# Kernel optimization log

Hardware: AMD Instinct MI355X
Metric: run time of the kernel (lower is better)

## Reference

```python
import jax, jax.numpy as jnp
import numpy as np

B, D, C, F = 1024, 8192, 345, 512
PROTO_W = 0.99  # args.proto_m


def setup_inputs() -> dict:
    key = jax.random.key(0)
    k = jax.random.split(key, 6)
    img_q = jax.random.normal(k[0], (B, D), jnp.float32)
    img_q1 = jax.random.normal(k[1], (B, D), jnp.float32)
    # partial label mask: random candidate set, guarantee >=1 candidate per row
    partial_Y = (jax.random.uniform(k[2], (B, C)) < 0.3).astype(jnp.float32)
    partial_Y = partial_Y.at[jnp.arange(B), jnp.arange(B) % C].set(1.0)
    W_enc = jax.random.normal(k[3], (D, F), jnp.float32) / np.sqrt(D).astype(np.float32)
    W_fc = jax.random.normal(k[4], (F, C), jnp.float32) / np.sqrt(F).astype(np.float32)
    b_fc = jnp.zeros((C,), jnp.float32)
    proto = jax.random.normal(k[5], (C, F), jnp.float32)
    proto = proto / jnp.linalg.norm(proto, axis=1, keepdims=True)
    return {"img_q": img_q, "img_q1": img_q1, "partial_Y": partial_Y,
            "W_enc": W_enc, "W_fc": W_fc, "b_fc": b_fc, "proto": proto}


def reference(img_q, img_q1, partial_Y, W_enc, W_fc, b_fc, proto):
    # encoder: feats [B,F], logits [B,C] (abstracted backbone + shared fc)
    feats_q = img_q @ W_enc
    logits_q = feats_q @ W_fc + b_fc
    feats_q1 = img_q1 @ W_enc
    logits_q1 = feats_q1 @ W_fc + b_fc

    # partial-label restricted pseudo labels
    scores = jax.nn.softmax(logits_q, axis=1) * partial_Y
    scores = scores / scores.sum(axis=1, keepdims=True)
    labels = jnp.argmax(scores, axis=1)  # [B] int

    # Sequential per-sample EMA p[l] = w*p[l] + (1-w)*f, vectorized in closed form.
    # For a sample with c_after same-label samples occurring later, its final
    # contribution is (1-w)*w^c_after * f; the old prototype is scaled by w^count.
    onehot = jax.nn.one_hot(labels, C, dtype=feats_q.dtype)   # [B,C]
    cum = jnp.cumsum(onehot, axis=0)                          # inclusive counts
    occ = cum[jnp.arange(B), labels] - 1.0                    # occurrences before i
    total = cum[-1]                                           # [C] per-class counts
    c_after = total[labels] - occ - 1.0                       # [B]
    coef = (1.0 - PROTO_W) * PROTO_W ** c_after               # [B]
    contrib = jax.ops.segment_sum(coef[:, None] * feats_q, labels, num_segments=C)
    new_proto = (PROTO_W ** total)[:, None] * proto + contrib
    new_proto = new_proto / jnp.linalg.norm(new_proto, axis=1, keepdims=True)

    prot_scores = new_proto @ W_fc + b_fc
    return logits_q, logits_q1, new_proto, prot_scores, labels, feats_q, feats_q1
```

## Files before the change

### kernel.cpp

```cpp
#include <hip/hip_runtime.h>
#include <float.h>
#include <math.h>

#define B_SZ 1024
#define D_SZ 8192
#define C_SZ 345
#define F_SZ 512
#define PROTO_W 0.99f


#define WS_XH 0
#define WS_XL 33554432u
#define WS_WH 67108864u
#define WS_WL 75497472u
#define WS_P  83886080u
#define WS2_WFH 100663296u
#define WS2_WFL 101056512u
#define WS2_LAB 101449728u
#define WS2_NEED 101457920u
#define WS2_FH 0u
#define WS2_FL 2097152u

#define WS_NEED 92274688u
#define WS_FH  0u
#define WS_FL  2097152u
#define WS_WFH 4194304u
#define WS_WFL 4587520u
#define WS_NPH 4980736u
#define WS_NPL 5373952u

typedef short bf16x8 __attribute__((ext_vector_type(8)));
typedef short short4v __attribute__((ext_vector_type(4)));
typedef short short8v __attribute__((ext_vector_type(8)));
typedef float f32x4  __attribute__((ext_vector_type(4)));

__device__ __forceinline__ void split_bf16(float x, short& hi, short& lo) {
    unsigned u = __float_as_uint(x);
    unsigned r = (u + 0x7FFFu + ((u >> 16) & 1u)) >> 16;
    hi = (short)r;
    float hf = __uint_as_float(r << 16);
    lo = (short)(__float_as_uint(x - hf) >> 16);
}
__device__ __forceinline__ float bf16_f32(short h) {
    return __uint_as_float(((unsigned)(unsigned short)h) << 16);
}

__device__ __forceinline__ void gl_lds16(const short* g, short* l) {
    __builtin_amdgcn_global_load_lds(
        (const __attribute__((address_space(1))) void*)g,
        (__attribute__((address_space(3))) void*)l, 16, 0, 0);
}

__device__ __forceinline__ unsigned f2key(float v) {
    unsigned u = __float_as_uint(v);
    return (u & 0x80000000u) ? ~u : (u | 0x80000000u);
}

__device__ __forceinline__ void fence_barrier() {
    asm volatile("" ::: "memory");
    __builtin_amdgcn_s_barrier();
    asm volatile("" ::: "memory");
}

#define MFMA_BF16 __builtin_amdgcn_mfma_f32_16x16x32_bf16

#define MFMA_BLOCK(IA0, IA1, IB0, IB1)                                   \
    do {                                                                 \
        bf16x8 a0h = *(const bf16x8*)&sAh[IA0];                          \
        bf16x8 a1h = *(const bf16x8*)&sAh[IA1];                          \
        bf16x8 b0h = *(const bf16x8*)&sBh[IB0];                          \
        bf16x8 b1h = *(const bf16x8*)&sBh[IB1];                          \
        bf16x8 a0l = *(const bf16x8*)&sAl[IA0];                          \
        bf16x8 a1l = *(const bf16x8*)&sAl[IA1];                          \
        bf16x8 b0l = *(const bf16x8*)&sBl[IB0];                          \
        bf16x8 b1l = *(const bf16x8*)&sBl[IB1];                          \
        acc[0][0] = MFMA_BF16(a0h, b0h, acc[0][0], 0, 0, 0);             \
        acc[0][1] = MFMA_BF16(a0h, b1h, acc[0][1], 0, 0, 0);             \
        acc[1][0] = MFMA_BF16(a1h, b0h, acc[1][0], 0, 0, 0);             \
        acc[1][1] = MFMA_BF16(a1h, b1h, acc[1][1], 0, 0, 0);             \
        acc[0][0] = MFMA_BF16(a0h, b0l, acc[0][0], 0, 0, 0);             \
        acc[0][1] = MFMA_BF16(a0h, b1l, acc[0][1], 0, 0, 0);             \
        acc[1][0] = MFMA_BF16(a1h, b0l, acc[1][0], 0, 0, 0);             \
        acc[1][1] = MFMA_BF16(a1h, b1l, acc[1][1], 0, 0, 0);             \
        acc[0][0] = MFMA_BF16(a0l, b0h, acc[0][0], 0, 0, 0);             \
        acc[0][1] = MFMA_BF16(a0l, b1h, acc[0][1], 0, 0, 0);             \
        acc[1][0] = MFMA_BF16(a1l, b0h, acc[1][0], 0, 0, 0);             \
        acc[1][1] = MFMA_BF16(a1l, b1h, acc[1][1], 0, 0, 0);             \
    } while (0)

__global__ __launch_bounds__(256) void convert_all(
    const float* __restrict__ img_q, const float* __restrict__ img_q1,
    const float* __restrict__ W_enc, const float* __restrict__ W_fc,
    short* __restrict__ Xh, short* __restrict__ Xl,
    short* __restrict__ Wh, short* __restrict__ Wl,
    short* __restrict__ Wth, short* __restrict__ Wtl)
{
    __shared__ float tile[64][65];
    const int bid = blockIdx.x;
    const int t = threadIdx.x;

    if (bid < 1024) {
        const int HALF = (B_SZ * D_SZ) / 4;
        const int total = 2 * HALF;
        for (int i4 = bid * 256 + t; i4 < total; i4 += 1024 * 256) {
            float4 v = (i4 < HALF) ? ((const float4*)img_q)[i4]
                                   : ((const float4*)img_q1)[i4 - HALF];
            short4v h, l;
            short hh, ll;
            split_bf16(v.x, hh, ll); h.x = hh; l.x = ll;
            split_bf16(v.y, hh, ll); h.y = hh; l.y = ll;
            split_bf16(v.z, hh, ll); h.z = hh; l.z = ll;
            split_bf16(v.w, hh, ll); h.w = hh; l.w = ll;
            ((short4v*)Xh)[i4] = h;
            ((short4v*)Xl)[i4] = l;
        }
    } else if (bid < 2048) {
        const int id = bid - 1024;
        const int k0 = (id >> 3) * 64;
        const int n0 = (id & 7) * 64;
        {
            const int kr = t >> 2;
            const int cb = (t & 3) * 16;
#pragma unroll
            for (int j = 0; j < 4; ++j) {
                float4 v = *(const float4*)&W_enc[(size_t)(k0 + kr) * F_SZ + n0 + cb + j * 4];
                tile[kr][cb + j * 4 + 0] = v.x;
                tile[kr][cb + j * 4 + 1] = v.y;
                tile[kr][cb + j * 4 + 2] = v.z;
                tile[kr][cb + j * 4 + 3] = v.w;
            }
        }
        __syncthreads();
        const int n = t >> 2;
#pragma unroll
        for (int cc = 0; cc < 2; ++cc) {
            const int ch = (t & 3) * 2 + cc;
            short8v h, l;
#pragma unroll
            for (int e = 0; e < 8; ++e) {
                short hh, ll;
                split_bf16(tile[ch * 8 + e][n], hh, ll);
                h[e] = hh; l[e] = ll;
            }
            size_t off = (size_t)(n0 + n) * D_SZ + k0 + ch * 8;
            *(short8v*)&Wh[off] = h;
            *(short8v*)&Wl[off] = l;
        }
    } else {
        const int id = bid - 2048;
        const int k0 = (id & 7) * 64;
        const int c0 = (id >> 3) * 64;
        for (int idx = t; idx < 64 * 64; idx += 256) {
            const int kr = idx >> 6;
            const int cc = idx & 63;
            tile[kr][cc] = (c0 + cc < C_SZ) ? W_fc[(size_t)(k0 + kr) * C_SZ + c0 + cc] : 0.0f;
        }
        __syncthreads();
        const int crow = t >> 2;
#pragma unroll
        for (int cc2 = 0; cc2 < 2; ++cc2) {
            const int ch = (t & 3) * 2 + cc2;
            short8v h, l;
#pragma unroll
            for (int e = 0; e < 8; ++e) {
                short hh, ll;
                split_bf16(tile[ch * 8 + e][crow], hh, ll);
                h[e] = hh; l[e] = ll;
            }
            size_t off = (size_t)(c0 + crow) * F_SZ + k0 + ch * 8;
            *(short8v*)&Wth[off] = h;
            *(short8v*)&Wtl[off] = l;
        }
    }
}

__global__ __launch_bounds__(512, 1) void gemm_ws128_v3(
    const short* __restrict__ Xh, const short* __restrict__ Xl,
    const short* __restrict__ Wh, const short* __restrict__ Wl,
    float* __restrict__ P, int ksteps)
{
    __shared__ __align__(16) short sAh[2][8192];
    __shared__ __align__(16) short sAl[2][8192];
    __shared__ __align__(16) short sBh[2][8192];
    __shared__ __align__(16) short sBl[2][8192];

    const int t = threadIdx.x;
    const int lane = t & 63;
    const int wave = t >> 6;

    const int flat = blockIdx.x + 4 * blockIdx.y + 64 * blockIdx.z;
    const int logical = (flat & 7) * 32 + (flat >> 3);
    const int nt = logical & 3;
    const int mt = (logical >> 2) & 15;
    const int ks = logical >> 6;

    const int m0 = mt * 128;
    const int n0 = nt * 128;
    const int kbase = ks * ksteps * 64;

    const int arr = wave >> 1;
    const int half = wave & 1;
    const short* gbase =
        (arr == 0) ? Xh + (size_t)m0 * D_SZ :
        (arr == 1) ? Xl + (size_t)m0 * D_SZ :
        (arr == 2) ? Wh + (size_t)n0 * D_SZ :
                     Wl + (size_t)n0 * D_SZ;
    short* lb[2];
    lb[0] = ((arr == 0) ? sAh[0] : (arr == 1) ? sAl[0] : (arr == 2) ? sBh[0] : sBl[0]) + half * 4096;
    lb[1] = ((arr == 0) ? sAh[1] : (arr == 1) ? sAl[1] : (arr == 2) ? sBh[1] : sBl[1]) + half * 4096;
    const int lrow8 = lane >> 3;
    const int gchunkOff = ((lane & 7) ^ lrow8) * 8;
    const short* gsrc = gbase + (size_t)(half * 64 + lrow8) * D_SZ + kbase + gchunkOff;

    const int wr = wave >> 2;
    const int wc = wave & 3;
    const int mo = wr * 64;
    const int no = wc * 32;
    const int lr = lane & 15;
    const int lkg = lane >> 4;
    const int x7 = lr & 7;
    const int sl0 = lkg ^ x7;
    const int sl1 = (4 + lkg) ^ x7;
    int aoff[4], boff[2];
#pragma unroll
    for (int f = 0; f < 4; ++f) aoff[f] = (mo + 16 * f + lr) * 64;
#pragma unroll
    for (int g = 0; g < 2; ++g) boff[g] = (no + 16 * g + lr) * 64;

    f32x4 acc[4][2] = {};

#pragma unroll
    for (int j = 0; j < 8; ++j)
        gl_lds16(gsrc + (size_t)(8 * j) * D_SZ, lb[0] + j * 512);

    int buf = 0;
    for (int s = 0; s < ksteps; ++s) {
        if (s + 1 < ksteps) {
            short* dst = lb[buf ^ 1];
            const short* g = gsrc + (s + 1) * 64;
#pragma unroll
            for (int j = 0; j < 8; ++j)
                gl_lds16(g + (size_t)(8 * j) * D_SZ, dst + j * 512);
            asm volatile("s_waitcnt vmcnt(8)" ::: "memory");
        } else {
            asm volatile("s_waitcnt vmcnt(0)" ::: "memory");
        }
        fence_barrier();

        const short* pAh = sAh[buf];
        const short* pAl = sAl[buf];
        const short* pBh = sBh[buf];
        const short* pBl = sBl[buf];

        {
            bf16x8 ah[4], al[4], bh[2], bl_[2];
#pragma unroll
            for (int f = 0; f < 4; ++f) {
                ah[f] = *(const bf16x8*)&pAh[aoff[f] + sl0 * 8];
                al[f] = *(const bf16x8*)&pAl[aoff[f] + sl0 * 8];
            }
#pragma unroll
            for (int g = 0; g < 2; ++g) {
                bh[g]  = *(const bf16x8*)&pBh[boff[g] + sl0 * 8];
                bl_[g] = *(const bf16x8*)&pBl[boff[g] + sl0 * 8];
            }
            __builtin_amdgcn_s_setprio(1);
#pragma unroll
            for (int f = 0; f < 4; ++f)
#pragma unroll
                for (int g = 0; g < 2; ++g)
                    acc[f][g] = MFMA_BF16(ah[f], bh[g], acc[f][g], 0, 0, 0);
#pragma unroll
            for (int f = 0; f < 4; ++f)
#pragma unroll
                for (int g = 0; g < 2; ++g)
                    acc[f][g] = MFMA_BF16(ah[f], bl_[g], acc[f][g], 0, 0, 0);
#pragma unroll
            for (int f = 0; f < 4; ++f)
#pragma unroll
                for (int g = 0; g < 2; ++g)
                    acc[f][g] = MFMA_BF16(al[f], bh[g], acc[f][g], 0, 0, 0);
            __builtin_amdgcn_s_setprio(0);
        }
        fence_barrier();

        {
            bf16x8 ah[4], al[4], bh[2], bl_[2];
#pragma unroll
            for (int f = 0; f < 4; ++f) {
                ah[f] = *(const bf16x8*)&pAh[aoff[f] + sl1 * 8];
                al[f] = *(const bf16x8*)&pAl[aoff[f] + sl1 * 8];
            }
#pragma unroll
            for (int g = 0; g < 2; ++g) {
                bh[g]  = *(const bf16x8*)&pBh[boff[g] + sl1 * 8];
                bl_[g] = *(const bf16x8*)&pBl[boff[g] + sl1 * 8];
            }
            __builtin_amdgcn_s_setprio(1);
#pragma unroll
            for (int f = 0; f < 4; ++f)
#pragma unroll
                for (int g = 0; g < 2; ++g)
                    acc[f][g] = MFMA_BF16(ah[f], bh[g], acc[f][g], 0, 0, 0);
#pragma unroll
            for (int f = 0; f < 4; ++f)
#pragma unroll
                for (int g = 0; g < 2; ++g)
                    acc[f][g] = MFMA_BF16(ah[f], bl_[g], acc[f][g], 0, 0, 0);
#pragma unroll
            for (int f = 0; f < 4; ++f)
#pragma unroll
                for (int g = 0; g < 2; ++g)
                    acc[f][g] = MFMA_BF16(al[f], bh[g], acc[f][g], 0, 0, 0);
            __builtin_amdgcn_s_setprio(0);
        }
        fence_barrier();
        buf ^= 1;
    }

    float* Pout = P + (size_t)ks * (2048u * 512u);
#pragma unroll
    for (int f = 0; f < 4; ++f)
#pragma unroll
        for (int g = 0; g < 2; ++g) {
            const int col  = n0 + no + 16 * g + (lane & 15);
            const int row0 = m0 + mo + 16 * f + (lane >> 4) * 4;
#pragma unroll
            for (int r = 0; r < 4; ++r)
                Pout[(size_t)(row0 + r) * F_SZ + col] = acc[f][g][r];
        }
}

__global__ __launch_bounds__(256, 1) void gemm_ws128(
    const short* __restrict__ Xh, const short* __restrict__ Xl,
    const short* __restrict__ Wh, const short* __restrict__ Wl,
    float* __restrict__ P, int ksteps)
{
    __shared__ __align__(16) short sAh[2][8192];
    __shared__ __align__(16) short sAl[2][8192];
    __shared__ __align__(16) short sBh[2][8192];
    __shared__ __align__(16) short sBl[2][8192];

    const int t = threadIdx.x;
    const int lane = t & 63;
    const int wave = t >> 6;
    const int nt = blockIdx.x;
    const int mt = blockIdx.y;
    const int ks = blockIdx.z;
    const int m0 = mt * 128;
    const int n0 = nt * 128;
    const int kbase = ks * ksteps * 64;

    const short* gbase =
        (wave == 0) ? Xh + (size_t)m0 * D_SZ :
        (wave == 1) ? Xl + (size_t)m0 * D_SZ :
        (wave == 2) ? Wh + (size_t)n0 * D_SZ :
                      Wl + (size_t)n0 * D_SZ;
    short* lb[2];
    lb[0] = (wave == 0) ? sAh[0] : (wave == 1) ? sAl[0] : (wave == 2) ? sBh[0] : sBl[0];
    lb[1] = (wave == 0) ? sAh[1] : (wave == 1) ? sAl[1] : (wave == 2) ? sBh[1] : sBl[1];
    const int lrow8 = lane >> 3;
    const int gchunkOff = ((lane & 7) ^ lrow8) * 8;
    const short* gsrc = gbase + (size_t)lrow8 * D_SZ + kbase + gchunkOff;

    const int mo = (wave >> 1) * 64;
    const int no = (wave & 1) * 64;
    const int lr = lane & 15;
    const int lkg = lane >> 4;
    const int x7 = lr & 7;
    const int sl0 = lkg ^ x7;
    const int sl1 = (4 + lkg) ^ x7;
    int aoff[4], boff[4];
#pragma unroll
    for (int f = 0; f < 4; ++f) {
        aoff[f] = (mo + 16 * f + lr) * 64;
        boff[f] = (no + 16 * f + lr) * 64;
    }

    f32x4 acc[4][4] = {};

#pragma unroll
    for (int j = 0; j < 16; ++j)
        gl_lds16(gsrc + (size_t)(8 * j) * D_SZ, lb[0] + j * 512);

    int buf = 0;
    for (int s = 0; s < ksteps; ++s) {
        if (s + 1 < ksteps) {
            short* dst = lb[buf ^ 1];
            const short* g = gsrc + (s + 1) * 64;
#pragma unroll
            for (int j = 0; j < 16; ++j)
                gl_lds16(g + (size_t)(8 * j) * D_SZ, dst + j * 512);
            asm volatile("s_waitcnt vmcnt(16)" ::: "memory");
        } else {
            asm volatile("s_waitcnt vmcnt(0)" ::: "memory");
        }
        fence_barrier();

        __builtin_amdgcn_s_setprio(1);
        {
            const short* pAh = sAh[buf];
            const short* pAl = sAl[buf];
            const short* pBh = sBh[buf];
            const short* pBl = sBl[buf];
#pragma unroll
            for (int ksub = 0; ksub < 2; ++ksub) {
                const int sl = ksub ? sl1 : sl0;
                bf16x8 ah[4], al[4], bh[4], blo[4];
#pragma unroll
                for (int f = 0; f < 4; ++f) {
                    ah[f]  = *(const bf16x8*)&pAh[aoff[f] + sl * 8];
                    al[f]  = *(const bf16x8*)&pAl[aoff[f] + sl * 8];
                }
#pragma unroll
                for (int g = 0; g < 4; ++g) {
                    bh[g]  = *(const bf16x8*)&pBh[boff[g] + sl * 8];
                    blo[g] = *(const bf16x8*)&pBl[boff[g] + sl * 8];
                }
#pragma unroll
                for (int f = 0; f < 4; ++f)
#pragma unroll
                    for (int g = 0; g < 4; ++g)
                        acc[f][g] = MFMA_BF16(ah[f], bh[g], acc[f][g], 0, 0, 0);
#pragma unroll
                for (int f = 0; f < 4; ++f)
#pragma unroll
                    for (int g = 0; g < 4; ++g)
                        acc[f][g] = MFMA_BF16(ah[f], blo[g], acc[f][g], 0, 0, 0);
#pragma unroll
                for (int f = 0; f < 4; ++f)
#pragma unroll
                    for (int g = 0; g < 4; ++g)
                        acc[f][g] = MFMA_BF16(al[f], bh[g], acc[f][g], 0, 0, 0);
            }
        }
        __builtin_amdgcn_s_setprio(0);
        fence_barrier();
        buf ^= 1;
    }

    float* Pout = P + (size_t)ks * (2048u * 512u);
#pragma unroll
    for (int f = 0; f < 4; ++f)
#pragma unroll
        for (int g = 0; g < 4; ++g) {
            const int col  = n0 + no + 16 * g + (lane & 15);
            const int row0 = m0 + mo + 16 * f + (lane >> 4) * 4;
#pragma unroll
            for (int r = 0; r < 4; ++r)
                Pout[(size_t)(row0 + r) * F_SZ + col] = acc[f][g][r];
        }
}

__global__ __launch_bounds__(256) void reduce_feats4(
    const float* __restrict__ P, float* __restrict__ feats,
    short* __restrict__ Fh, short* __restrict__ Fl)
{
    const int i4 = blockIdx.x * 256 + threadIdx.x;
    float4 a = ((const float4*)P)[i4];
#pragma unroll
    for (int sl = 1; sl < 4; ++sl) {
        float4 b = ((const float4*)(P + (size_t)sl * (2048u * 512u)))[i4];
        a.x += b.x; a.y += b.y; a.z += b.z; a.w += b.w;
    }
    ((float4*)feats)[i4] = a;
    float v[4] = {a.x, a.y, a.z, a.w};
    short4v h, l;
    short hh, ll;
#pragma unroll
    for (int e = 0; e < 4; ++e) {
        split_bf16(v[e], hh, ll); h[e] = hh; l[e] = ll;
    }
    ((short4v*)Fh)[i4] = h;
    ((short4v*)Fl)[i4] = l;
}

__global__ __launch_bounds__(256, 2) void fc_logits3(
    const short* __restrict__ Ah, const short* __restrict__ Al,
    const short* __restrict__ Bh_g, const short* __restrict__ Bl_g,
    const float* __restrict__ bias, const float* __restrict__ partial_Y,
    float* __restrict__ logits, unsigned long long* __restrict__ labPack)
{
    __shared__ __align__(16) short dAh[2][4096];
    __shared__ __align__(16) short dAl[2][4096];
    __shared__ __align__(16) short dBh[2][4096];
    __shared__ __align__(16) short dBl[2][4096];

    const int t = threadIdx.x;
    const int lane = t & 63;
    const int wave = t >> 6;
    const int n0 = blockIdx.x * 64;
    const int m0 = blockIdx.y * 64;

    const int lrow8 = lane >> 3;
    const int colOff = ((lane & 7) ^ lrow8) * 8;

    const short* gsrc = (wave == 0) ? Ah : (wave == 1) ? Al
                      : (wave == 2) ? Bh_g : Bl_g;
    const int rbase = (wave < 2) ? m0 : n0;
    short* lb[2];
    lb[0] = (wave == 0) ? dAh[0] : (wave == 1) ? dAl[0] : (wave == 2) ? dBh[0] : dBl[0];
    lb[1] = (wave == 0) ? dAh[1] : (wave == 1) ? dAl[1] : (wave == 2) ? dBh[1] : dBl[1];
    const short* gbase = gsrc + (size_t)(rbase + lrow8) * F_SZ + colOff;

    const int mo = (wave >> 1) * 32;
    const int no = (wave & 1) * 32;
    const int lr = lane & 15;
    const int lkg = lane >> 4;
    const int x7 = lr & 7;
    const int sl0 = (0 + lkg) ^ x7;
    const int sl1 = (4 + lkg) ^ x7;
    const int ra0 = (mo + lr) * 64,      ra1 = (mo + 16 + lr) * 64;
    const int rb0 = (no + lr) * 64,      rb1 = (no + 16 + lr) * 64;
    const int a00 = ra0 + sl0 * 8, a01 = ra0 + sl1 * 8;
    const int a10 = ra1 + sl0 * 8, a11 = ra1 + sl1 * 8;
    const int b00 = rb0 + sl0 * 8, b01 = rb0 + sl1 * 8;
    const int b10 = rb1 + sl0 * 8, b11 = rb1 + sl1 * 8;

    f32x4 acc[2][2] = {};

#pragma unroll
    for (int j = 0; j < 8; ++j)
        gl_lds16(gbase + (size_t)(8 * j) * F_SZ, lb[0] + j * 512);

    int buf = 0;
    for (int s = 0; s < 8; ++s) {
        if (s + 1 < 8) {
            short* dst = lb[buf ^ 1];
            const short* g = gbase + (s + 1) * 64;
#pragma unroll
            for (int j = 0; j < 8; ++j)
                gl_lds16(g + (size_t)(8 * j) * F_SZ, dst + j * 512);
            asm volatile("s_waitcnt vmcnt(8)" ::: "memory");
        } else {
            asm volatile("s_waitcnt vmcnt(0)" ::: "memory");
        }
        fence_barrier();
        __builtin_amdgcn_s_setprio(1);
        {
            const short* sAh = dAh[buf];
            const short* sAl = dAl[buf];
            const short* sBh = dBh[buf];
            const short* sBl = dBl[buf];
            MFMA_BLOCK(a00, a10, b00, b10);
            MFMA_BLOCK(a01, a11, b01, b11);
        }
        __builtin_amdgcn_s_setprio(0);
        fence_barrier();
        buf ^= 1;
    }

    const bool doArg = (m0 < B_SZ);
#pragma unroll
    for (int f = 0; f < 2; ++f) {
#pragma unroll
        for (int r = 0; r < 4; ++r) {
            const int row = m0 + mo + f * 16 + (lane >> 4) * 4 + r;
            unsigned long long best = 0;
#pragma unroll
            for (int g = 0; g < 2; ++g) {
                const int col = n0 + no + g * 16 + (lane & 15);
                if (col < C_SZ) {
                    const float v = acc[f][g][r] + bias[col];
                    logits[(size_t)row * C_SZ + col] = v;
                    if (doArg && partial_Y[(size_t)row * C_SZ + col] != 0.0f) {
                        unsigned long long p = ((unsigned long long)f2key(v) << 32)
                                             | (unsigned long long)(0xFFFFFFFFu - (unsigned)col);
                        if (p > best) best = p;
                    }
                }
            }
            if (doArg) {
#pragma unroll
                for (int m = 1; m < 16; m <<= 1) {
                    unsigned long long o = __shfl_xor(best, m);
                    if (o > best) best = o;
                }
                if ((lane & 15) == 0 && best != 0)
                    atomicMax(&labPack[row], best);
            }
        }
    }
}

__global__ __launch_bounds__(512) void proto_scores_fused(
    const unsigned long long* __restrict__ labPack,
    const float* __restrict__ feats_q,
    const float* __restrict__ proto,
    const short* __restrict__ Wth, const short* __restrict__ Wtl,
    const float* __restrict__ b_fc,
    float* __restrict__ new_proto, float* __restrict__ scores,
    float* __restrict__ labels_f)
{
    __shared__ int rowlist[B_SZ];
    __shared__ int mcount_s;
    __shared__ float nprow[F_SZ];
    __shared__ float red[8];
    __shared__ float rinv_s;
    const int c = blockIdx.x;
    const int t = threadIdx.x;
    const int lane = t & 63;
    const int w = t >> 6;

    if (c == 0) {
#pragma unroll
        for (int j = 0; j < 2; ++j) {
            const int i = t + j * 512;
            int li = (int)(0xFFFFFFFFu - (unsigned)(labPack[i] & 0xFFFFFFFFull));
            labels_f[i] = (float)li;
        }
    }

    if (w == 0) {
        int k = 0;
#pragma unroll
        for (int ch = 0; ch < 16; ++ch) {
            unsigned long long pk = labPack[ch * 64 + lane];
            int li = (int)(0xFFFFFFFFu - (unsigned)(pk & 0xFFFFFFFFull));
            unsigned long long mask = __ballot(li == c);
            if (lane == 0) {
                while (mask) {
                    int p = __builtin_ctzll(mask);
                    mask &= mask - 1;
                    rowlist[k++] = ch * 64 + p;
                }
            }
            k = __shfl(k, 0);
        }
        if (lane == 0) mcount_s = k;
    }
    __syncthreads();
    const int m = mcount_s;

    float val = proto[(size_t)c * F_SZ + t];
    for (int k = 0; k < m; ++k)
        val = PROTO_W * val + (1.0f - PROTO_W) * feats_q[(size_t)rowlist[k] * F_SZ + t];

    float sq = val * val;
#pragma unroll
    for (int off = 32; off; off >>= 1) sq += __shfl_down(sq, off);
    if ((t & 63) == 0) red[t >> 6] = sq;
    __syncthreads();
    if (t == 0) {
        float s = 0.0f;
#pragma unroll
        for (int ww = 0; ww < 8; ++ww) s += red[ww];
        rinv_s = 1.0f / sqrtf(s);
    }
    __syncthreads();
    const float v = val * rinv_s;
    new_proto[(size_t)c * F_SZ + t] = v;
    nprow[t] = v;
    __syncthreads();

    float np8[8];
#pragma unroll
    for (int j = 0; j < 8; ++j) np8[j] = nprow[lane * 8 + j];
    for (int col = w; col < C_SZ; col += 8) {
        const short8v h = *(const short8v*)&Wth[(size_t)col * F_SZ + lane * 8];
        const short8v l = *(const short8v*)&Wtl[(size_t)col * F_SZ + lane * 8];
        float p = 0.0f;
#pragma unroll
        for (int j = 0; j < 8; ++j)
            p += np8[j] * (bf16_f32(h[j]) + bf16_f32(l[j]));
#pragma unroll
        for (int off = 32; off; off >>= 1) p += __shfl_down(p, off);
        if (lane == 0) scores[(size_t)c * C_SZ + col] = p + b_fc[col];
    }
}

__global__ __launch_bounds__(256) void reduce_feats_split(
    const float* __restrict__ P, float* __restrict__ feats,
    short* __restrict__ Fh, short* __restrict__ Fl,
    const float* __restrict__ W_fc,
    short* __restrict__ Wth, short* __restrict__ Wtl)
{
    const int bid = blockIdx.x;
    const int t = threadIdx.x;
    if (bid < 1024) {
        const int n4 = (2048 * 512) / 4;
        const float* P1 = P + 2048 * 512;
        for (int i4 = bid * 256 + t; i4 < n4; i4 += 1024 * 256) {
            float4 a = ((const float4*)P)[i4];
            float4 b = ((const float4*)P1)[i4];
            float v[4] = {a.x + b.x, a.y + b.y, a.z + b.z, a.w + b.w};
            short4v h, l;
            short hh, ll;
#pragma unroll
            for (int e = 0; e < 4; ++e) {
                feats[i4 * 4 + e] = v[e];
                split_bf16(v[e], hh, ll); h[e] = hh; l[e] = ll;
            }
            ((short4v*)Fh)[i4] = h;
            ((short4v*)Fl)[i4] = l;
        }
    } else {
        __shared__ float tile[64][65];
        const int id = bid - 1024;
        const int k0 = (id & 7) * 64;
        const int c0 = (id >> 3) * 64;
        for (int idx = t; idx < 64 * 64; idx += 256) {
            const int kr = idx >> 6;
            const int cc = idx & 63;
            tile[kr][cc] = (c0 + cc < C_SZ) ? W_fc[(size_t)(k0 + kr) * C_SZ + c0 + cc] : 0.0f;
        }
        __syncthreads();
        const int crow = t >> 2;
#pragma unroll
        for (int cc2 = 0; cc2 < 2; ++cc2) {
            const int ch = (t & 3) * 2 + cc2;
            short8v h, l;
#pragma unroll
            for (int e = 0; e < 8; ++e) {
                short hh, ll;
                split_bf16(tile[ch * 8 + e][crow], hh, ll);
                h[e] = hh; l[e] = ll;
            }
            size_t off = (size_t)(c0 + crow) * F_SZ + k0 + ch * 8;
            *(short8v*)&Wth[off] = h;
            *(short8v*)&Wtl[off] = l;
        }
    }
}

__global__ __launch_bounds__(256) void gemm_fc(
    const short* __restrict__ Ah, const short* __restrict__ Al,
    const short* __restrict__ Bh, const short* __restrict__ Bl,
    const float* __restrict__ bias, float* __restrict__ Cout, int M)
{
    __shared__ __align__(16) short sAh[4096];
    __shared__ __align__(16) short sAl[4096];
    __shared__ __align__(16) short sBh[4096];
    __shared__ __align__(16) short sBl[4096];

    const int t = threadIdx.x;
    const int lane = t & 63;
    const int wave = t >> 6;
    const int n0 = blockIdx.x * 64;
    const int m0 = blockIdx.y * 64;

    const int lrow8 = lane >> 3;
    const int colOff = ((lane & 7) ^ lrow8) * 8;

    short* lbase = (wave == 0) ? sAh : (wave == 1) ? sAl : (wave == 2) ? sBh : sBl;
    const short* gA = (wave == 1) ? Al : Ah;
    const short* gB = (wave == 3) ? Bl : Bh;
    const bool isA = wave < 2;

    const int mo = (wave >> 1) * 32;
    const int no = (wave & 1) * 32;
    const int lr = lane & 15;
    const int lkg = lane >> 4;
    const int x7 = lr & 7;
    const int sl0 = (0 + lkg) ^ x7;
    const int sl1 = (4 + lkg) ^ x7;
    const int ra0 = (mo + lr) * 64,      ra1 = (mo + 16 + lr) * 64;
    const int rb0 = (no + lr) * 64,      rb1 = (no + 16 + lr) * 64;
    const int a00 = ra0 + sl0 * 8, a01 = ra0 + sl1 * 8;
    const int a10 = ra1 + sl0 * 8, a11 = ra1 + sl1 * 8;
    const int b00 = rb0 + sl0 * 8, b01 = rb0 + sl1 * 8;
    const int b10 = rb1 + sl0 * 8, b11 = rb1 + sl1 * 8;

    f32x4 acc[2][2] = {};

    for (int s = 0; s < 8; ++s) {
        __syncthreads();
        if (isA) {
#pragma unroll
            for (int j = 0; j < 8; ++j) {
                int row = m0 + lrow8 + 8 * j;
                if (row > M - 1) row = M - 1;
                gl_lds16(gA + (size_t)row * F_SZ + s * 64 + colOff, lbase + j * 512);
            }
        } else {
#pragma unroll
            for (int j = 0; j < 8; ++j) {
                int row = n0 + lrow8 + 8 * j;
                gl_lds16(gB + (size_t)row * F_SZ + s * 64 + colOff, lbase + j * 512);
            }
        }
        __syncthreads();
        MFMA_BLOCK(a00, a10, b00, b10);
        MFMA_BLOCK(a01, a11, b01, b11);
    }

#pragma unroll
    for (int f = 0; f < 2; ++f)
#pragma unroll
        for (int g = 0; g < 2; ++g) {
            const int col  = n0 + no + g * 16 + (lane & 15);
            if (col >= C_SZ) continue;
            const float bb = bias[col];
            const int row0 = m0 + mo + f * 16 + (lane >> 4) * 4;
#pragma unroll
            for (int r = 0; r < 4; ++r) {
                const int row = row0 + r;
                if (row < M)
                    Cout[(size_t)row * C_SZ + col] = acc[f][g][r] + bb;
            }
        }
}

__global__ __launch_bounds__(64) void argmax_labels(
    const float* __restrict__ logits, const float* __restrict__ partial_Y,
    float* __restrict__ labels_f)
{
    const int i = blockIdx.x;
    const int lane = threadIdx.x;
    float best = -FLT_MAX;
    int bidx = C_SZ;
    for (int c = lane; c < C_SZ; c += 64) {
        if (partial_Y[(size_t)i * C_SZ + c] != 0.0f) {
            float v = logits[(size_t)i * C_SZ + c];
            if (v > best || (v == best && c < bidx)) { best = v; bidx = c; }
        }
    }
#pragma unroll
    for (int off = 32; off; off >>= 1) {
        float ov = __shfl_down(best, off);
        int oi = __shfl_down(bidx, off);
        if (ov > best || (ov == best && oi < bidx)) { best = ov; bidx = oi; }
    }
    if (lane == 0) labels_f[i] = (float)bidx;
}

__global__ __launch_bounds__(512) void proto_update(
    const float* __restrict__ labels_f, const float* __restrict__ feats_q,
    const float* __restrict__ proto, float* __restrict__ new_proto,
    short* __restrict__ NPh, short* __restrict__ NPl)
{
    __shared__ int lab[B_SZ];
    __shared__ float red[8];
    __shared__ float rinv_s;
    const int c = blockIdx.x;
    const int t = threadIdx.x;
    for (int i = t; i < B_SZ; i += 512) lab[i] = (int)labels_f[i];
    __syncthreads();
    float val = proto[(size_t)c * F_SZ + t];
    for (int i = 0; i < B_SZ; ++i) {
        if (lab[i] == c)
            val = PROTO_W * val + (1.0f - PROTO_W) * feats_q[(size_t)i * F_SZ + t];
    }
    float sq = val * val;
#pragma unroll
    for (int off = 32; off; off >>= 1) sq += __shfl_down(sq, off);
    if ((t & 63) == 0) red[t >> 6] = sq;
    __syncthreads();
    if (t == 0) {
        float s = 0.0f;
#pragma unroll
        for (int w = 0; w < 8; ++w) s += red[w];
        rinv_s = 1.0f / sqrtf(s);
    }
    __syncthreads();
    const float v = val * rinv_s;
    new_proto[(size_t)c * F_SZ + t] = v;
    if (NPh) {
        short hh, ll;
        split_bf16(v, hh, ll);
        NPh[(size_t)c * F_SZ + t] = hh;
        NPl[(size_t)c * F_SZ + t] = ll;
    }
}

extern "C" void kernel_launch(void* const* d_in, const int* in_sizes, int n_in,
                              void* d_out, int out_size, void* d_ws, size_t ws_size,
                              hipStream_t stream)
{
    const float* img_q     = (const float*)d_in[0];
    const float* img_q1    = (const float*)d_in[1];
    const float* partial_Y = (const float*)d_in[2];
    const float* W_enc     = (const float*)d_in[3];
    const float* W_fc      = (const float*)d_in[4];
    const float* b_fc      = (const float*)d_in[5];
    const float* proto     = (const float*)d_in[6];

    float* out       = (float*)d_out;
    float* logits    = out;
    float* new_proto = out + 706560;
    float* scores    = out + 883200;
    float* labels_f  = out + 1002225;
    float* feats     = out + 1003249;

    char* ws = (char*)d_ws;
    short* Xh = (short*)(ws + WS_XH);
    short* Xl = (short*)(ws + WS_XL);
    short* Wh = (short*)(ws + WS_WH);
    short* Wl = (short*)(ws + WS_WL);
    float* P  = (float*)(ws + WS_P);

    if (ws_size >= (size_t)WS2_NEED) {
        short* Wth = (short*)(ws + WS2_WFH);
        short* Wtl = (short*)(ws + WS2_WFL);
        unsigned long long* labPack = (unsigned long long*)(ws + WS2_LAB);
        short* Fh = (short*)(ws + WS2_FH);
        short* Fl = (short*)(ws + WS2_FL);

        hipMemsetAsync(labPack, 0, B_SZ * sizeof(unsigned long long), stream);
        hipLaunchKernelGGL(convert_all, dim3(2096), dim3(256), 0, stream,
                           img_q, img_q1, W_enc, W_fc, Xh, Xl, Wh, Wl, Wth, Wtl);
        hipLaunchKernelGGL(gemm_ws128_v3, dim3(4, 16, 4), dim3(512), 0, stream,
                           Xh, Xl, Wh, Wl, P, 32);
        hipLaunchKernelGGL(reduce_feats4, dim3(1024), dim3(256), 0, stream,
                           P, feats, Fh, Fl);
        hipLaunchKernelGGL(fc_logits3, dim3(6, 32), dim3(256), 0, stream,
                           Fh, Fl, Wth, Wtl, b_fc, partial_Y, logits, labPack);
        hipLaunchKernelGGL(proto_scores_fused, dim3(345), dim3(512), 0, stream,
                           labPack, feats, proto, Wth, Wtl, b_fc,
                           new_proto, scores, labels_f);
    } else {
        short* Fh  = (short*)(ws + WS_FH);
        short* Fl  = (short*)(ws + WS_FL);
        short* Wth = (short*)(ws + WS_WFH);
        short* Wtl = (short*)(ws + WS_WFL);
        short* NPh = (short*)(ws + WS_NPH);
        short* NPl = (short*)(ws + WS_NPL);

        hipLaunchKernelGGL(convert_all, dim3(2048), dim3(256), 0, stream,
                           img_q, img_q1, W_enc, W_fc, Xh, Xl, Wh, Wl,
                           (short*)nullptr, (short*)nullptr);
        hipLaunchKernelGGL(gemm_ws128, dim3(4, 16, 2), dim3(256), 0, stream,
                           Xh, Xl, Wh, Wl, P, 64);
        hipLaunchKernelGGL(reduce_feats_split, dim3(1072), dim3(256), 0, stream,
                           P, feats, Fh, Fl, W_fc, Wth, Wtl);
        hipLaunchKernelGGL(gemm_fc, dim3(6, 32), dim3(256), 0, stream,
                           Fh, Fl, Wth, Wtl, b_fc, logits, 2048);
        hipLaunchKernelGGL(argmax_labels, dim3(1024), dim3(64), 0, stream,
                           logits, partial_Y, labels_f);
        hipLaunchKernelGGL(proto_update, dim3(345), dim3(512), 0, stream,
                           labels_f, feats, proto, new_proto, NPh, NPl);
        hipLaunchKernelGGL(gemm_fc, dim3(6, 6), dim3(256), 0, stream,
                           NPh, NPl, Wth, Wtl, b_fc, scores, C_SZ);
    }
}
```

Baseline: 248.2 us.

## Fuse split-K reduction into fc logits GEMM and fold labPack zeroing into convert

The separate split-K reduction kernel and the fc logits GEMM are merged into one kernel. Each block of 32 rows sums the four partial slices, writes feats, splits them to bf16 hi/lo straight into LDS, and then loops over all six class tiles with double-buffered W_fc loads. The labPack memset is moved into the first blocks of convert_all, which removes one launch and the Fh/Fl round trip through global memory. In exchange the fused kernel runs only 64 blocks, so GPU occupancy is much lower and the A-side reduction is serialized with the MFMA work.

```diff
diff --git a/kernel.cpp b/kernel.cpp
--- a/kernel.cpp
+++ b/kernel.cpp
@@ -18,8 +18,6 @@
 #define WS2_WFL 101056512u
 #define WS2_LAB 101449728u
 #define WS2_NEED 101457920u
-#define WS2_FH 0u
-#define WS2_FL 2097152u
 
 #define WS_NEED 92274688u
 #define WS_FH  0u
@@ -93,11 +91,15 @@
     const float* __restrict__ W_enc, const float* __restrict__ W_fc,
     short* __restrict__ Xh, short* __restrict__ Xl,
     short* __restrict__ Wh, short* __restrict__ Wl,
-    short* __restrict__ Wth, short* __restrict__ Wtl)
+    short* __restrict__ Wth, short* __restrict__ Wtl,
+    unsigned long long* __restrict__ labPack)
 {
     __shared__ float tile[64][65];
     const int bid = blockIdx.x;
     const int t = threadIdx.x;
+
+    if (labPack && bid < 4)
+        labPack[bid * 256 + t] = 0ull;
 
     if (bid < 1024) {
         const int HALF = (B_SZ * D_SZ) / 4;
@@ -452,39 +454,308 @@
         }
 }
 
-__global__ __launch_bounds__(256) void reduce_feats4(
+__device__ __forceinline__ void prep_A(
     const float* __restrict__ P, float* __restrict__ feats,
-    short* __restrict__ Fh, short* __restrict__ Fl)
-{
-    const int i4 = blockIdx.x * 256 + threadIdx.x;
-    float4 a = ((const float4*)P)[i4];
+    int m0, int s, int t, short* sAh_, short* sAl_)
+{
+    const int ar = t >> 3;
+    const int ac = t & 7;
+    const size_t gidx = (size_t)(m0 + ar) * F_SZ + s * 64 + ac * 8;
+    float4 v0 = ((const float4*)&P[gidx])[0];
+    float4 v1 = ((const float4*)&P[gidx])[1];
 #pragma unroll
     for (int sl = 1; sl < 4; ++sl) {
-        float4 b = ((const float4*)(P + (size_t)sl * (2048u * 512u)))[i4];
-        a.x += b.x; a.y += b.y; a.z += b.z; a.w += b.w;
-    }
-    ((float4*)feats)[i4] = a;
-    float v[4] = {a.x, a.y, a.z, a.w};
-    short4v h, l;
-    short hh, ll;
-#pragma unroll
-    for (int e = 0; e < 4; ++e) {
-        split_bf16(v[e], hh, ll); h[e] = hh; l[e] = ll;
-    }
-    ((short4v*)Fh)[i4] = h;
-    ((short4v*)Fl)[i4] = l;
-}
-
-__global__ __launch_bounds__(256, 2) void fc_logits3(
-    const short* __restrict__ Ah, const short* __restrict__ Al,
-    const short* __restrict__ Bh_g, const short* __restrict__ Bl_g,
+        const float* Ps = P + (size_t)sl * (2048u * 512u);
+        float4 u0 = ((const float4*)&Ps[gidx])[0];
+        float4 u1 = ((const float4*)&Ps[gidx])[1];
+        v0.x += u0.x; v0.y += u0.y; v0.z += u0.z; v0.w += u0.w;
+        v1.x += u1.x; v1.y += u1.y; v1.z += u1.z; v1.w += u1.w;
+    }
+    ((float4*)&feats[gidx])[0] = v0;
+    ((float4*)&feats[gidx])[1] = v1;
+    float f[8] = {v0.x, v0.y, v0.z, v0.w, v1.x, v1.y, v1.z, v1.w};
+    bf16x8 h, l;
+#pragma unroll
+    for (int e = 0; e < 8; ++e) {
+        short hh, ll;
+        split_bf16(f[e], hh, ll);
+        h[e] = hh; l[e] = ll;
+    }
+    const int slot = ac ^ (ar & 7);
+    *(bf16x8*)&sAh_[ar * 64 + slot * 8] = h;
+    *(bf16x8*)&sAl_[ar * 64 + slot * 8] = l;
+    asm volatile("s_waitcnt lgkmcnt(0)" ::: "memory");
+}
+
+__global__ __launch_bounds__(256, 2) void fc_reduce_logits(
+    const float* __restrict__ P,
+    const short* __restrict__ Wth, const short* __restrict__ Wtl,
     const float* __restrict__ bias, const float* __restrict__ partial_Y,
-    float* __restrict__ logits, unsigned long long* __restrict__ labPack)
-{
-    __shared__ __align__(16) short dAh[2][4096];
-    __shared__ __align__(16) short dAl[2][4096];
+    float* __restrict__ logits, float* __restrict__ feats,
+    unsigned long long* __restrict__ labPack)
+{
+    __shared__ __align__(16) short sAh_[2048];
+    __shared__ __align__(16) short sAl_[2048];
     __shared__ __align__(16) short dBh[2][4096];
     __shared__ __align__(16) short dBl[2][4096];
+
+    const int t = threadIdx.x;
+    const int lane = t & 63;
+    const int wave = t >> 6;
+    const int m0 = blockIdx.x * 32;
+
+    const int lrow8 = lane >> 3;
+    const int colOff = ((lane & 7) ^ lrow8) * 8;
+    const short* gB = (wave < 2) ? Wth : Wtl;
+    const int jbase = (wave & 1) * 4;
+
+    const int mo = (wave >> 1) * 16;
+    const int no_w = (wave & 1) * 32;
+    const int lr = lane & 15;
+    const int lkg = lane >> 4;
+    const int x7 = lr & 7;
+    const int sl0 = lkg ^ x7;
+    const int sl1 = (4 + lkg) ^ x7;
+    const int arow = (mo + lr) * 64;
+    const int brow0 = (no_w + lr) * 64;
+    const int brow1 = (no_w + 16 + lr) * 64;
+
+    f32x4 acc[6][2] = {};
+
+    {
+        short* dst = ((wave < 2) ? dBh[0] : dBl[0]) + jbase * 512;
+#pragma unroll
+        for (int jj = 0; jj < 4; ++jj)
+            gl_lds16(gB + (size_t)(8 * (jbase + jj) + lrow8) * F_SZ + colOff,
+                     dst + jj * 512);
+    }
+    prep_A(P, feats, m0, 0, t, sAh_, sAl_);
+
+    int buf = 0;
+    for (int s = 0; s < 8; ++s) {
+#pragma unroll
+        for (int nt = 0; nt < 6; ++nt) {
+            if (s < 7 || nt < 5) {
+                const int nt2 = (nt + 1) % 6;
+                const int s2 = s + ((nt == 5) ? 1 : 0);
+                short* dst = ((wave < 2) ? dBh[buf ^ 1] : dBl[buf ^ 1]) + jbase * 512;
+#pragma unroll
+                for (int jj = 0; jj < 4; ++jj)
+                    gl_lds16(gB + (size_t)(nt2 * 64 + 8 * (jbase + jj) + lrow8) * F_SZ + s2 * 64 + colOff,
+                             dst + jj * 512);
+                asm volatile("s_waitcnt vmcnt(4)" ::: "memory");
+            } else {
+                asm volatile("s_waitcnt vmcnt(0)" ::: "memory");
+            }
+            fence_barrier();
+            const short* pBh = dBh[buf];
+            const short* pBl = dBl[buf];
+            __builtin_amdgcn_s_setprio(1);
+#pragma unroll
+            for (int ksub = 0; ksub < 2; ++ksub) {
+                const int sl = ksub ? sl1 : sl0;
+                bf16x8 a_h = *(const bf16x8*)&sAh_[arow + sl * 8];
+                bf16x8 a_l = *(const bf16x8*)&sAl_[arow + sl * 8];
+                bf16x8 b0h = *(const bf16x8*)&pBh[brow0 + sl * 8];
+                bf16x8 b1h = *(const bf16x8*)&pBh[brow1 + sl * 8];
+                bf16x8 b0l = *(const bf16x8*)&pBl[brow0 + sl * 8];
+                bf16x8 b1l = *(const bf16x8*)&pBl[brow1 + sl * 8];
+                acc[nt][0] = MFMA_BF16(a_h, b0h, acc[nt][0], 0, 0, 0);
+                acc[nt][1] = MFMA_BF16(a_h, b1h, acc[nt][1], 0, 0, 0);
+                acc[nt][0] = MFMA_BF16(a_h, b0l, acc[nt][0], 0, 0, 0);
+                acc[nt][1] = MFMA_BF16(a_h, b1l, acc[nt][1], 0, 0, 0);
+                acc[nt][0] = MFMA_BF16(a_l, b0h, acc[nt][0], 0, 0, 0);
+                acc[nt][1] = MFMA_BF16(a_l, b1h, acc[nt][1], 0, 0, 0);
+            }
+            __builtin_amdgcn_s_setprio(0);
+            fence_barrier();
+            buf ^= 1;
+        }
+        if (s < 7)
+            prep_A(P, feats, m0, s + 1, t, sAh_, sAl_);
+    }
+
+    const bool doArg = (m0 < B_SZ);
+#pragma unroll
+    for (int r = 0; r < 4; ++r) {
+        const int row = m0 + mo + lkg * 4 + r;
+        unsigned long long best = 0;
+#pragma unroll
+        for (int nt = 0; nt < 6; ++nt)
+#pragma unroll
+            for (int g = 0; g < 2; ++g) {
+                const int col = nt * 64 + no_w + g * 16 + lr;
+                if (col < C_SZ) {
+                    const float v = acc[nt][g][r] + bias[col];
+                    logits[(size_t)row * C_SZ + col] = v;
+                    if (doArg && partial_Y[(size_t)row * C_SZ + col] != 0.0f) {
+                        unsigned long long pk = ((unsigned long long)f2key(v) << 32)
+                                              | (unsigned long long)(0xFFFFFFFFu - (unsigned)col);
+                        if (pk > best) best = pk;
+                    }
+                }
+            }
+        if (doArg) {
+#pragma unroll
+            for (int mm = 1; mm < 16; mm <<= 1) {
+                unsigned long long o = __shfl_xor(best, mm);
+                if (o > best) best = o;
+            }
+            if (lr == 0 && best != 0)
+                atomicMax(&labPack[row], best);
+        }
+    }
+}
+
+__global__ __launch_bounds__(512) void proto_scores_fused(
+    const unsigned long long* __restrict__ labPack,
+    const float* __restrict__ feats_q,
+    const float* __restrict__ proto,
+    const short* __restrict__ Wth, const short* __restrict__ Wtl,
+    const float* __restrict__ b_fc,
+    float* __restrict__ new_proto, float* __restrict__ scores,
+    float* __restrict__ labels_f)
+{
+    __shared__ int rowlist[B_SZ];
+    __shared__ int mcount_s;
+    __shared__ float nprow[F_SZ];
+    __shared__ float red[8];
+    __shared__ float rinv_s;
+    const int c = blockIdx.x;
+    const int t = threadIdx.x;
+    const int lane = t & 63;
+    const int w = t >> 6;
+
+    if (c == 0) {
+#pragma unroll
+        for (int j = 0; j < 2; ++j) {
+            const int i = t + j * 512;
+            int li = (int)(0xFFFFFFFFu - (unsigned)(labPack[i] & 0xFFFFFFFFull));
+            labels_f[i] = (float)li;
+        }
+    }
+
+    if (w == 0) {
+        int k = 0;
+#pragma unroll
+        for (int ch = 0; ch < 16; ++ch) {
+            unsigned long long pk = labPack[ch * 64 + lane];
+            int li = (int)(0xFFFFFFFFu - (unsigned)(pk & 0xFFFFFFFFull));
+            unsigned long long mask = __ballot(li == c);
+            if (lane == 0) {
+                while (mask) {
+                    int p = __builtin_ctzll(mask);
+                    mask &= mask - 1;
+                    rowlist[k++] = ch * 64 + p;
+                }
+            }
+            k = __shfl(k, 0);
+        }
+        if (lane == 0) mcount_s = k;
+    }
+    __syncthreads();
+    const int m = mcount_s;
+
+    float val = proto[(size_t)c * F_SZ + t];
+    for (int k = 0; k < m; ++k)
+        val = PROTO_W * val + (1.0f - PROTO_W) * feats_q[(size_t)rowlist[k] * F_SZ + t];
+
+    float sq = val * val;
+#pragma unroll
+    for (int off = 32; off; off >>= 1) sq += __shfl_down(sq, off);
+    if ((t & 63) == 0) red[t >> 6] = sq;
+    __syncthreads();
+    if (t == 0) {
+        float s = 0.0f;
+#pragma unroll
+        for (int ww = 0; ww < 8; ++ww) s += red[ww];
+        rinv_s = 1.0f / sqrtf(s);
+    }
+    __syncthreads();
+    const float v = val * rinv_s;
+    new_proto[(size_t)c * F_SZ + t] = v;
+    nprow[t] = v;
+    __syncthreads();
+
+    float np8[8];
+#pragma unroll
+    for (int j = 0; j < 8; ++j) np8[j] = nprow[lane * 8 + j];
+    for (int col = w; col < C_SZ; col += 8) {
+        const short8v h = *(const short8v*)&Wth[(size_t)col * F_SZ + lane * 8];
+        const short8v l = *(const short8v*)&Wtl[(size_t)col * F_SZ + lane * 8];
+        float p = 0.0f;
+#pragma unroll
+        for (int j = 0; j < 8; ++j)
+            p += np8[j] * (bf16_f32(h[j]) + bf16_f32(l[j]));
+#pragma unroll
+        for (int off = 32; off; off >>= 1) p += __shfl_down(p, off);
+        if (lane == 0) scores[(size_t)c * C_SZ + col] = p + b_fc[col];
+    }
+}
+
+__global__ __launch_bounds__(256) void reduce_feats_split(
+    const float* __restrict__ P, float* __restrict__ feats,
+    short* __restrict__ Fh, short* __restrict__ Fl,
+    const float* __restrict__ W_fc,
+    short* __restrict__ Wth, short* __restrict__ Wtl)
+{
+    const int bid = blockIdx.x;
+    const int t = threadIdx.x;
+    if (bid < 1024) {
+        const int n4 = (2048 * 512) / 4;
+        const float* P1 = P + 2048 * 512;
+        for (int i4 = bid * 256 + t; i4 < n4; i4 += 1024 * 256) {
+            float4 a = ((const float4*)P)[i4];
+            float4 b = ((const float4*)P1)[i4];
+            float v[4] = {a.x + b.x, a.y + b.y, a.z + b.z, a.w + b.w};
+            short4v h, l;
+            short hh, ll;
+#pragma unroll
+            for (int e = 0; e < 4; ++e) {
+                feats[i4 * 4 + e] = v[e];
+                split_bf16(v[e], hh, ll); h[e] = hh; l[e] = ll;
+            }
+            ((short4v*)Fh)[i4] = h;
+            ((short4v*)Fl)[i4] = l;
+        }
+    } else {
+        __shared__ float tile[64][65];
+        const int id = bid - 1024;
+        const int k0 = (id & 7) * 64;
+        const int c0 = (id >> 3) * 64;
+        for (int idx = t; idx < 64 * 64; idx += 256) {
+            const int kr = idx >> 6;
+            const int cc = idx & 63;
+            tile[kr][cc] = (c0 + cc < C_SZ) ? W_fc[(size_t)(k0 + kr) * C_SZ + c0 + cc] : 0.0f;
+        }
+        __syncthreads();
+        const int crow = t >> 2;
+#pragma unroll
+        for (int cc2 = 0; cc2 < 2; ++cc2) {
+            const int ch = (t & 3) * 2 + cc2;
+            short8v h, l;
+#pragma unroll
+            for (int e = 0; e < 8; ++e) {
+                short hh, ll;
+                split_bf16(tile[ch * 8 + e][crow], hh, ll);
+                h[e] = hh; l[e] = ll;
+            }
+            size_t off = (size_t)(c0 + crow) * F_SZ + k0 + ch * 8;
+            *(short8v*)&Wth[off] = h;
+            *(short8v*)&Wtl[off] = l;
+        }
+    }
+}
+
+__global__ __launch_bounds__(256) void gemm_fc(
+    const short* __restrict__ Ah, const short* __restrict__ Al,
+    const short* __restrict__ Bh, const short* __restrict__ Bl,
+    const float* __restrict__ bias, float* __restrict__ Cout, int M)
+{
+    __shared__ __align__(16) short sAh[4096];
+    __shared__ __align__(16) short sAl[4096];
+    __shared__ __align__(16) short sBh[4096];
+    __shared__ __align__(16) short sBl[4096];
 
     const int t = threadIdx.x;
     const int lane = t & 63;
@@ -495,13 +766,10 @@
     const int lrow8 = lane >> 3;
     const int colOff = ((lane & 7) ^ lrow8) * 8;
 
-    const short* gsrc = (wave == 0) ? Ah : (wave == 1) ? Al
-                      : (wave == 2) ? Bh_g : Bl_g;
-    const int rbase = (wave < 2) ? m0 : n0;
-    short* lb[2];
-    lb[0] = (wave == 0) ? dAh[0] : (wave == 1) ? dAl[0] : (wave == 2) ? dBh[0] : dBl[0];
-    lb[1] = (wave == 0) ? dAh[1] : (wave == 1) ? dAl[1] : (wave == 2) ? dBh[1] : dBl[1];
-    const short* gbase = gsrc + (size_t)(rbase + lrow8) * F_SZ + colOff;
+    short* lbase = (wave == 0) ? sAh : (wave == 1) ? sAl : (wave == 2) ? sBh : sBl;
+    const short* gA = (wave == 1) ? Al : Ah;
+    const short* gB = (wave == 3) ? Bl : Bh;
+    const bool isA = wave < 2;
 
     const int mo = (wave >> 1) * 32;
     const int no = (wave & 1) * 32;
@@ -519,250 +787,6 @@
 
     f32x4 acc[2][2] = {};
 
-#pragma unroll
-    for (int j = 0; j < 8; ++j)
-        gl_lds16(gbase + (size_t)(8 * j) * F_SZ, lb[0] + j * 512);
-
-    int buf = 0;
-    for (int s = 0; s < 8; ++s) {
-        if (s + 1 < 8) {
-            short* dst = lb[buf ^ 1];
-            const short* g = gbase + (s + 1) * 64;
-#pragma unroll
-            for (int j = 0; j < 8; ++j)
-                gl_lds16(g + (size_t)(8 * j) * F_SZ, dst + j * 512);
-            asm volatile("s_waitcnt vmcnt(8)" ::: "memory");
-        } else {
-            asm volatile("s_waitcnt vmcnt(0)" ::: "memory");
-        }
-        fence_barrier();
-        __builtin_amdgcn_s_setprio(1);
-        {
-            const short* sAh = dAh[buf];
-            const short* sAl = dAl[buf];
-            const short* sBh = dBh[buf];
-            const short* sBl = dBl[buf];
-            MFMA_BLOCK(a00, a10, b00, b10);
-            MFMA_BLOCK(a01, a11, b01, b11);
-        }
-        __builtin_amdgcn_s_setprio(0);
-        fence_barrier();
-        buf ^= 1;
-    }
-
-    const bool doArg = (m0 < B_SZ);
-#pragma unroll
-    for (int f = 0; f < 2; ++f) {
-#pragma unroll
-        for (int r = 0; r < 4; ++r) {
-            const int row = m0 + mo + f * 16 + (lane >> 4) * 4 + r;
-            unsigned long long best = 0;
-#pragma unroll
-            for (int g = 0; g < 2; ++g) {
-                const int col = n0 + no + g * 16 + (lane & 15);
-                if (col < C_SZ) {
-                    const float v = acc[f][g][r] + bias[col];
-                    logits[(size_t)row * C_SZ + col] = v;
-                    if (doArg && partial_Y[(size_t)row * C_SZ + col] != 0.0f) {
-                        unsigned long long p = ((unsigned long long)f2key(v) << 32)
-                                             | (unsigned long long)(0xFFFFFFFFu - (unsigned)col);
-                        if (p > best) best = p;
-                    }
-                }
-            }
-            if (doArg) {
-#pragma unroll
-                for (int m = 1; m < 16; m <<= 1) {
-                    unsigned long long o = __shfl_xor(best, m);
-                    if (o > best) best = o;
-                }
-                if ((lane & 15) == 0 && best != 0)
-                    atomicMax(&labPack[row], best);
-            }
-        }
-    }
-}
-
-__global__ __launch_bounds__(512) void proto_scores_fused(
-    const unsigned long long* __restrict__ labPack,
-    const float* __restrict__ feats_q,
-    const float* __restrict__ proto,
-    const short* __restrict__ Wth, const short* __restrict__ Wtl,
-    const float* __restrict__ b_fc,
-    float* __restrict__ new_proto, float* __restrict__ scores,
-    float* __restrict__ labels_f)
-{
-    __shared__ int rowlist[B_SZ];
-    __shared__ int mcount_s;
-    __shared__ float nprow[F_SZ];
-    __shared__ float red[8];
-    __shared__ float rinv_s;
-    const int c = blockIdx.x;
-    const int t = threadIdx.x;
-    const int lane = t & 63;
-    const int w = t >> 6;
-
-    if (c == 0) {
-#pragma unroll
-        for (int j = 0; j < 2; ++j) {
-            const int i = t + j * 512;
-            int li = (int)(0xFFFFFFFFu - (unsigned)(labPack[i] & 0xFFFFFFFFull));
-            labels_f[i] = (float)li;
-        }
-    }
-
-    if (w == 0) {
-        int k = 0;
-#pragma unroll
-        for (int ch = 0; ch < 16; ++ch) {
-            unsigned long long pk = labPack[ch * 64 + lane];
-            int li = (int)(0xFFFFFFFFu - (unsigned)(pk & 0xFFFFFFFFull));
-            unsigned long long mask = __ballot(li == c);
-            if (lane == 0) {
-                while (mask) {
-                    int p = __builtin_ctzll(mask);
-                    mask &= mask - 1;
-                    rowlist[k++] = ch * 64 + p;
-                }
-            }
-            k = __shfl(k, 0);
-        }
-        if (lane == 0) mcount_s = k;
-    }
-    __syncthreads();
-    const int m = mcount_s;
-
-    float val = proto[(size_t)c * F_SZ + t];
-    for (int k = 0; k < m; ++k)
-        val = PROTO_W * val + (1.0f - PROTO_W) * feats_q[(size_t)rowlist[k] * F_SZ + t];
-
-    float sq = val * val;
-#pragma unroll
-    for (int off = 32; off; off >>= 1) sq += __shfl_down(sq, off);
-    if ((t & 63) == 0) red[t >> 6] = sq;
-    __syncthreads();
-    if (t == 0) {
-        float s = 0.0f;
-#pragma unroll
-        for (int ww = 0; ww < 8; ++ww) s += red[ww];
-        rinv_s = 1.0f / sqrtf(s);
-    }
-    __syncthreads();
-    const float v = val * rinv_s;
-    new_proto[(size_t)c * F_SZ + t] = v;
-    nprow[t] = v;
-    __syncthreads();
-
-    float np8[8];
-#pragma unroll
-    for (int j = 0; j < 8; ++j) np8[j] = nprow[lane * 8 + j];
-    for (int col = w; col < C_SZ; col += 8) {
-        const short8v h = *(const short8v*)&Wth[(size_t)col * F_SZ + lane * 8];
-        const short8v l = *(const short8v*)&Wtl[(size_t)col * F_SZ + lane * 8];
-        float p = 0.0f;
-#pragma unroll
-        for (int j = 0; j < 8; ++j)
-            p += np8[j] * (bf16_f32(h[j]) + bf16_f32(l[j]));
-#pragma unroll
-        for (int off = 32; off; off >>= 1) p += __shfl_down(p, off);
-        if (lane == 0) scores[(size_t)c * C_SZ + col] = p + b_fc[col];
-    }
-}
-
-__global__ __launch_bounds__(256) void reduce_feats_split(
-    const float* __restrict__ P, float* __restrict__ feats,
-    short* __restrict__ Fh, short* __restrict__ Fl,
-    const float* __restrict__ W_fc,
-    short* __restrict__ Wth, short* __restrict__ Wtl)
-{
-    const int bid = blockIdx.x;
-    const int t = threadIdx.x;
-    if (bid < 1024) {
-        const int n4 = (2048 * 512) / 4;
-        const float* P1 = P + 2048 * 512;
-        for (int i4 = bid * 256 + t; i4 < n4; i4 += 1024 * 256) {
-            float4 a = ((const float4*)P)[i4];
-            float4 b = ((const float4*)P1)[i4];
-            float v[4] = {a.x + b.x, a.y + b.y, a.z + b.z, a.w + b.w};
-            short4v h, l;
-            short hh, ll;
-#pragma unroll
-            for (int e = 0; e < 4; ++e) {
-                feats[i4 * 4 + e] = v[e];
-                split_bf16(v[e], hh, ll); h[e] = hh; l[e] = ll;
-            }
-            ((short4v*)Fh)[i4] = h;
-            ((short4v*)Fl)[i4] = l;
-        }
-    } else {
-        __shared__ float tile[64][65];
-        const int id = bid - 1024;
-        const int k0 = (id & 7) * 64;
-        const int c0 = (id >> 3) * 64;
-        for (int idx = t; idx < 64 * 64; idx += 256) {
-            const int kr = idx >> 6;
-            const int cc = idx & 63;
-            tile[kr][cc] = (c0 + cc < C_SZ) ? W_fc[(size_t)(k0 + kr) * C_SZ + c0 + cc] : 0.0f;
-        }
-        __syncthreads();
-        const int crow = t >> 2;
-#pragma unroll
-        for (int cc2 = 0; cc2 < 2; ++cc2) {
-            const int ch = (t & 3) * 2 + cc2;
-            short8v h, l;
-#pragma unroll
-            for (int e = 0; e < 8; ++e) {
-                short hh, ll;
-                split_bf16(tile[ch * 8 + e][crow], hh, ll);
-                h[e] = hh; l[e] = ll;
-            }
-            size_t off = (size_t)(c0 + crow) * F_SZ + k0 + ch * 8;
-            *(short8v*)&Wth[off] = h;
-            *(short8v*)&Wtl[off] = l;
-        }
-    }
-}
-
-__global__ __launch_bounds__(256) void gemm_fc(
-    const short* __restrict__ Ah, const short* __restrict__ Al,
-    const short* __restrict__ Bh, const short* __restrict__ Bl,
-    const float* __restrict__ bias, float* __restrict__ Cout, int M)
-{
-    __shared__ __align__(16) short sAh[4096];
-    __shared__ __align__(16) short sAl[4096];
-    __shared__ __align__(16) short sBh[4096];
-    __shared__ __align__(16) short sBl[4096];
-
-    const int t = threadIdx.x;
-    const int lane = t & 63;
-    const int wave = t >> 6;
-    const int n0 = blockIdx.x * 64;
-    const int m0 = blockIdx.y * 64;
-
-    const int lrow8 = lane >> 3;
-    const int colOff = ((lane & 7) ^ lrow8) * 8;
-
-    short* lbase = (wave == 0) ? sAh : (wave == 1) ? sAl : (wave == 2) ? sBh : sBl;
-    const short* gA = (wave == 1) ? Al : Ah;
-    const short* gB = (wave == 3) ? Bl : Bh;
-    const bool isA = wave < 2;
-
-    const int mo = (wave >> 1) * 32;
-    const int no = (wave & 1) * 32;
-    const int lr = lane & 15;
-    const int lkg = lane >> 4;
-    const int x7 = lr & 7;
-    const int sl0 = (0 + lkg) ^ x7;
-    const int sl1 = (4 + lkg) ^ x7;
-    const int ra0 = (mo + lr) * 64,      ra1 = (mo + 16 + lr) * 64;
-    const int rb0 = (no + lr) * 64,      rb1 = (no + 16 + lr) * 64;
-    const int a00 = ra0 + sl0 * 8, a01 = ra0 + sl1 * 8;
-    const int a10 = ra1 + sl0 * 8, a11 = ra1 + sl1 * 8;
-    const int b00 = rb0 + sl0 * 8, b01 = rb0 + sl1 * 8;
-    const int b10 = rb1 + sl0 * 8, b11 = rb1 + sl1 * 8;
-
-    f32x4 acc[2][2] = {};
-
     for (int s = 0; s < 8; ++s) {
         __syncthreads();
         if (isA) {
@@ -893,18 +917,14 @@
         short* Wth = (short*)(ws + WS2_WFH);
         short* Wtl = (short*)(ws + WS2_WFL);
         unsigned long long* labPack = (unsigned long long*)(ws + WS2_LAB);
-        short* Fh = (short*)(ws + WS2_FH);
-        short* Fl = (short*)(ws + WS2_FL);
-
-        hipMemsetAsync(labPack, 0, B_SZ * sizeof(unsigned long long), stream);
+
         hipLaunchKernelGGL(convert_all, dim3(2096), dim3(256), 0, stream,
-                           img_q, img_q1, W_enc, W_fc, Xh, Xl, Wh, Wl, Wth, Wtl);
+                           img_q, img_q1, W_enc, W_fc, Xh, Xl, Wh, Wl, Wth, Wtl,
+                           labPack);
         hipLaunchKernelGGL(gemm_ws128_v3, dim3(4, 16, 4), dim3(512), 0, stream,
                            Xh, Xl, Wh, Wl, P, 32);
-        hipLaunchKernelGGL(reduce_feats4, dim3(1024), dim3(256), 0, stream,
-                           P, feats, Fh, Fl);
-        hipLaunchKernelGGL(fc_logits3, dim3(6, 32), dim3(256), 0, stream,
-                           Fh, Fl, Wth, Wtl, b_fc, partial_Y, logits, labPack);
+        hipLaunchKernelGGL(fc_reduce_logits, dim3(64), dim3(256), 0, stream,
+                           P, Wth, Wtl, b_fc, partial_Y, logits, feats, labPack);
         hipLaunchKernelGGL(proto_scores_fused, dim3(345), dim3(512), 0, stream,
                            labPack, feats, proto, Wth, Wtl, b_fc,
                            new_proto, scores, labels_f);
@@ -918,7 +938,8 @@
 
         hipLaunchKernelGGL(convert_all, dim3(2048), dim3(256), 0, stream,
                            img_q, img_q1, W_enc, W_fc, Xh, Xl, Wh, Wl,
-                           (short*)nullptr, (short*)nullptr);
+                           (short*)nullptr, (short*)nullptr,
+                           (unsigned long long*)nullptr);
         hipLaunchKernelGGL(gemm_ws128, dim3(4, 16, 2), dim3(256), 0, stream,
                            Xh, Xl, Wh, Wl, P, 64);
         hipLaunchKernelGGL(reduce_feats_split, dim3(1072), dim3(256), 0, stream,
```

Measured after the change: 266.5 us. 1.07x slower.
